# Kernel optimization log

Measured on AMD Instinct MI355X. Metric: run time of the kernel, lower is better.

## Reference

```python
import jax, jax.numpy as jnp
import numpy as np
import math

MAX_P = 150
D_MODEL = 128
N_HEADS = 4
D_HEAD = D_MODEL // N_HEADS
D_MLP = 512
D_MEM = 64
VOCAB = MAX_P + 2  # 152
EQ_TOKEN = MAX_P + 1  # 151
B = 65536


def setup_inputs() -> dict:
    key = jax.random.key(0)
    ks = jax.random.split(key, 20)
    s = 1.0 / math.sqrt(D_MODEL)
    inp = {
        "p_val": jax.random.randint(ks[0], (B,), 0, MAX_P),
        "a": jax.random.randint(ks[1], (B,), 0, MAX_P),
        "b": jax.random.randint(ks[2], (B,), 0, MAX_P),
        # embeddings
        "token_embed": jax.random.normal(ks[3], (VOCAB, D_MODEL), jnp.float32),
        "pos_embed": jax.random.normal(ks[4], (5, D_MODEL), jnp.float32),
        # TitansMemory
        "W_mem": jax.random.normal(ks[5], (D_MODEL, D_MEM), jnp.float32) * s,
        "b_mem": jnp.zeros((D_MEM,), jnp.float32),
        "W_sur": jax.random.normal(ks[6], (D_MEM, D_MODEL), jnp.float32) * (1.0 / math.sqrt(D_MEM)),
        "b_sur": jnp.zeros((D_MODEL,), jnp.float32),
        "W_m2r": jax.random.normal(ks[7], (D_MEM, D_MODEL), jnp.float32) * (1.0 / math.sqrt(D_MEM)),
        "b_m2r": jnp.zeros((D_MODEL,), jnp.float32),
        # attention
        "W_Q": jax.random.normal(ks[8], (N_HEADS, D_MODEL, D_HEAD), jnp.float32) * s,
        "W_K": jax.random.normal(ks[9], (N_HEADS, D_MODEL, D_HEAD), jnp.float32) * s,
        "W_V": jax.random.normal(ks[10], (N_HEADS, D_MODEL, D_HEAD), jnp.float32) * s,
        "W_O": jax.random.normal(ks[11], (N_HEADS, D_HEAD, D_MODEL), jnp.float32) * s,
        # MLP
        "W_mlp1": jax.random.normal(ks[12], (D_MODEL, D_MLP), jnp.float32) * s,
        "b_mlp1": jnp.zeros((D_MLP,), jnp.float32),
        "W_mlp2": jax.random.normal(ks[13], (D_MLP, D_MODEL), jnp.float32) * (1.0 / math.sqrt(D_MLP)),
        "b_mlp2": jnp.zeros((D_MODEL,), jnp.float32),
        # unembed
        "W_un": jax.random.normal(ks[14], (D_MODEL, MAX_P), jnp.float32) * s,
        "b_un": jnp.zeros((MAX_P,), jnp.float32),
    }
    return inp


def reference(p_val, a, b, token_embed, pos_embed, W_mem, b_mem, W_sur, b_sur,
              W_m2r, b_m2r, W_Q, W_K, W_V, W_O, W_mlp1, b_mlp1, W_mlp2, b_mlp2,
              W_un, b_un):
    eq = jnp.full_like(a, EQ_TOKEN)
    tokens = jnp.stack([p_val, a, b, eq], axis=1)            # [B, 4]
    x = token_embed[tokens] + pos_embed[:4][None, :, :]       # [B, 4, D]

    # Titans memory (test-time update) on the modulus token embedding
    x0 = x[:, 0, :]                                           # [B, D]
    z = jax.nn.silu(x0 @ W_mem + b_mem)                       # [B, d_mem]
    pred_x = z @ W_sur + b_sur                                # [B, D]
    update = jax.nn.silu((x0 - pred_x) @ W_mem)               # [B, d_mem]
    mem = (z + update) @ W_m2r + b_m2r                        # [B, D]
    x = x + mem[:, None, :]

    # attention
    q = jnp.einsum('bsd,hdk->bhsk', x, W_Q)
    k = jnp.einsum('bsd,hdk->bhsk', x, W_K)
    v = jnp.einsum('bsd,hdk->bhsk', x, W_V)
    scores = jnp.einsum('bhsk,bhtk->bhst', q, k) / math.sqrt(D_HEAD)
    pattern = jax.nn.softmax(scores, axis=-1)                 # [B, H, 4, 4]
    attn = jnp.einsum('bhst,bhtk->bhsk', pattern, v)
    attn = jnp.einsum('bhsk,hkm->bsm', attn, W_O)             # [B, 4, D]
    x = x + attn

    # MLP
    x = x + jax.nn.relu(x @ W_mlp1 + b_mlp1) @ W_mlp2 + b_mlp2

    # unembed the '=' position
    logits = x[:, 3, :] @ W_un + b_un                         # [B, max_p]
    return logits
```

## Files before the change

kernel.cpp:

```cpp
#include <hip/hip_runtime.h>

#define D      128
#define DM     64
#define DMLP   512
#define PMAX   150
#define VOC    152
#define EQT    151
#define NBATCH 65536

typedef __attribute__((ext_vector_type(8))) __bf16 bf16x8;
typedef __attribute__((ext_vector_type(4))) float  f32x4;

__device__ __forceinline__ float silu_f(float x){ return x / (1.0f + expf(-x)); }

#define OFF_MEMVEC 0
#define OFF_X3BASE 19200
#define OFF_KE     19328
#define OFF_KP     38784
#define OFF_SC     39296
#define OFF_O0     132896
#define OFF_O1     171296
#define OFF_O2     209696
#define OFF_O3     248096
#define OFF_M3B    248352
#define OFF_W1F    257952
#define OFF_W2F    290720
#define OFF_WUF    323488

__global__ void k_P1a(const float* __restrict__ tok, const float* __restrict__ pos,
                      const float* __restrict__ W_mem, const float* __restrict__ b_mem,
                      const float* __restrict__ W_sur, const float* __restrict__ b_sur,
                      const float* __restrict__ W_m2r, const float* __restrict__ b_m2r,
                      const float* __restrict__ W_K,
                      float* __restrict__ memvec, float* __restrict__ x3base,
                      float* __restrict__ KE, float* __restrict__ KP)
{
    int r = blockIdx.x, t = threadIdx.x;
    if (r < 150) {
        int p = r;
        __shared__ float sx0[D], sz[DM], sdiff[D], szu[DM];
        if (t < D) sx0[t] = tok[p*D + t] + pos[t];
        __syncthreads();
        if (t < DM) {
            float acc = b_mem[t];
            for (int d = 0; d < D; d++) acc += sx0[d] * W_mem[d*DM + t];
            sz[t] = silu_f(acc);
        }
        __syncthreads();
        if (t < D) {
            float acc = b_sur[t];
            for (int j = 0; j < DM; j++) acc += sz[j] * W_sur[j*D + t];
            sdiff[t] = sx0[t] - acc;
        }
        __syncthreads();
        if (t < DM) {
            float acc = 0.f;
            for (int d = 0; d < D; d++) acc += sdiff[d] * W_mem[d*DM + t];
            szu[t] = sz[t] + silu_f(acc);
        }
        __syncthreads();
        if (t < D) {
            float acc = b_m2r[t];
            for (int j = 0; j < DM; j++) acc += szu[j] * W_m2r[j*D + t];
            memvec[p*D + t] = acc;
        }
    } else if (r == 150) {
        if (t < D) x3base[t] = tok[EQT*D + t] + pos[3*D + t];
    } else {
        int idx = r - 151;
        const float* src = (idx < 152) ? (tok + idx*D) : (pos + (idx-152)*D);
        float*       dst = (idx < 152) ? (KE + idx*D)  : (KP + (idx-152)*D);
        __shared__ float s[D];
        if (t < D) s[t] = src[t];
        __syncthreads();
        if (t < D) {
            int h = t >> 5, k = t & 31;
            float acc = 0.f;
            for (int d = 0; d < D; d++) acc += s[d] * W_K[h*4096 + d*32 + k];
            dst[t] = acc;
        }
    }
}

__global__ void k_P2x(const float* __restrict__ memvec, const float* __restrict__ x3base,
                      const float* __restrict__ W_Q, const float* __restrict__ W_V,
                      const float* __restrict__ W_O,
                      const float* __restrict__ KE, const float* __restrict__ KP,
                      const float* __restrict__ tok, const float* __restrict__ pos,
                      const float* __restrict__ W1, const float* __restrict__ W2,
                      const float* __restrict__ WU,
                      float* __restrict__ SC, __bf16* __restrict__ M3B,
                      __bf16* __restrict__ O0, __bf16* __restrict__ O1,
                      __bf16* __restrict__ O2, __bf16* __restrict__ O3,
                      __bf16* __restrict__ W1f, __bf16* __restrict__ W2f, __bf16* __restrict__ WUf)
{
    int r = blockIdx.x, t = threadIdx.x;
    if (r < 300) {
        int p = r >> 1, half = r & 1;
        __shared__ float sMem[D], sIn[D], sQ3[D], sMV[D];
        if (t < D) { float m = memvec[p*D + t]; sMem[t] = m; sIn[t] = m + x3base[t]; }
        __syncthreads();
        if (t < D) {
            int h = t >> 5, k = t & 31;
            float acc = 0.f;
            for (int d = 0; d < D; d++) acc += sIn[d] * W_Q[h*4096 + d*32 + k];
            sQ3[t] = acc;
        } else {
            int c = t - D; int h = c >> 5, k = c & 31;
            float acc = 0.f;
            for (int d = 0; d < D; d++) acc += sMem[d] * W_V[h*4096 + d*32 + k];
            sMV[c] = acc;
        }
        __syncthreads();
        const float scale = 0.17677669529663687f;
        for (int ii = t; ii < 312; ii += 256) {
            int i = half*312 + ii;
            int v = i >> 2, h = i & 3;
            const float4* qh = (const float4*)(sQ3 + h*32);
            float4 s4 = {0.f, 0.f, 0.f, 0.f};
            if (v < 152) {
                const float4* ke = (const float4*)(KE + v*D + h*32);
                #pragma unroll
                for (int k = 0; k < 8; k++) {
                    float4 q = qh[k], e = ke[k];
                    s4.x += q.x*e.x; s4.y += q.y*e.y; s4.z += q.z*e.z; s4.w += q.w*e.w;
                }
            } else if (v == 152 || v == 153) {
                const float4* ke = (const float4*)(KE + ((v==152)? p : EQT)*D + h*32);
                const float4* kp = (const float4*)(KP + ((v==152)? 0 : 3)*D + h*32);
                #pragma unroll
                for (int k = 0; k < 8; k++) {
                    float4 q = qh[k], e = ke[k], pp = kp[k];
                    s4.x += q.x*(e.x+pp.x); s4.y += q.y*(e.y+pp.y);
                    s4.z += q.z*(e.z+pp.z); s4.w += q.w*(e.w+pp.w);
                }
            } else {
                const float4* kp = (const float4*)(KP + ((v==154)?1:2)*D + h*32);
                #pragma unroll
                for (int k = 0; k < 8; k++) {
                    float4 q = qh[k], pp = kp[k];
                    s4.x += q.x*pp.x; s4.y += q.y*pp.y; s4.z += q.z*pp.z; s4.w += q.w*pp.w;
                }
            }
            SC[p*624 + i] = (s4.x + s4.y + s4.z + s4.w) * scale;
        }
        if (half == 0 && t < D) {
            float acc = sIn[t];
            for (int c = 0; c < D; c++) acc += sMV[c] * W_O[c*D + t];
            M3B[p*D + t] = (__bf16)acc;
        }
        return;
    }
    int rr = r - 300;
    if (rr < 451) {
        int idx = rr;
        int tt, v; __bf16* outp;
        if (idx < 150)      { tt = 0; v = idx;       outp = O0 + v*512; }
        else if (idx < 300) { tt = 1; v = idx - 150; outp = O1 + (idx-150)*512; }
        else if (idx < 450) { tt = 2; v = idx - 300; outp = O2 + (idx-300)*512; }
        else                { tt = 3; v = EQT;       outp = O3; }
        __shared__ float sTP[D], sv[D];
        if (t < D) sTP[t] = tok[v*D + t] + pos[tt*D + t];
        __syncthreads();
        if (t < D) {
            int h = t >> 5, k = t & 31;
            float acc = 0.f;
            for (int d = 0; d < D; d++) acc += sTP[d] * W_V[h*4096 + d*32 + k];
            sv[t] = acc;
        }
        __syncthreads();
        #pragma unroll
        for (int i = 0; i < 2; i++) {
            int c = t + i*256;
            int h = c >> 7, m = c & 127;
            float acc = 0.f;
            for (int k = 0; k < 32; k++) acc += sv[h*32 + k] * W_O[h*4096 + k*128 + m];
            outp[c] = (__bf16)acc;
        }
    } else if (rr < 483) {
        int f = (rr-451)*256 + t;
        int l = f & 63, kb = (f>>6) & 3, nb = f >> 8;
        int k0 = kb*32 + (l>>4)*8, n = nb*16 + (l&15);
        #pragma unroll
        for (int j = 0; j < 8; j++) W1f[f*8 + j] = (__bf16)W1[(k0+j)*DMLP + n];
    } else if (rr < 515) {
        int f = (rr-483)*256 + t;
        int l = f & 63, g = f >> 6;
        int nb = g & 7, kb = g >> 3;
        int k0 = kb*32 + (l>>4)*8, n = nb*16 + (l&15);
        #pragma unroll
        for (int j = 0; j < 8; j++) W2f[f*8 + j] = (__bf16)W2[(k0+j)*D + n];
    } else {
        int f = (rr-515)*256 + t;
        int l = f & 63, kb = (f>>6) & 3, nb = f >> 8;
        int k0 = kb*32 + (l>>4)*8, n = nb*16 + (l&15);
        #pragma unroll
        for (int j = 0; j < 8; j++) WUf[f*8 + j] = (__bf16)((n < 150) ? WU[(k0+j)*150 + n] : 0.f);
    }
}

__global__ __launch_bounds__(256, 2) void k_fused(
    const int* __restrict__ p_val, const int* __restrict__ a_tok, const int* __restrict__ b_tok,
    const float* __restrict__ SC, const __bf16* __restrict__ O0, const __bf16* __restrict__ O1,
    const __bf16* __restrict__ O2, const __bf16* __restrict__ O3g, const __bf16* __restrict__ M3B,
    const __bf16* __restrict__ W1f, const __bf16* __restrict__ W2f, const __bf16* __restrict__ WUf,
    const float* __restrict__ b1, const float* __restrict__ b2, const float* __restrict__ bun,
    float* __restrict__ out)
{
    __shared__ __align__(16) char smem[54400];
    float* sB = (float*)(smem + 51200);
    char* sX3 = smem;

    int tid = threadIdx.x;
    int wv = tid >> 6, l = tid & 63, lr = l & 15, quad = l >> 4;
    int tbase = blockIdx.x * 128 + wv * 32;

    const char* gW1 = (const char*)W1f;
    const char* gW2 = (const char*)W2f;

    float4 v0, v1, v2, v3;
    {
        const float4* g1 = (const float4*)gW1;
        const float4* g2 = (const float4*)gW2;
        v0 = g1[tid]; v1 = g1[tid + 256]; v2 = g2[tid]; v3 = g2[tid + 256];
    }

    for (int i = tid; i < 512; i += 256) sB[i] = b1[i];
    if (tid < 128) sB[512 + tid] = b2[tid];
    if (tid < 160) sB[640 + tid] = bun[tid];

    #pragma unroll
    for (int ss = 0; ss < 2; ss++) {
        int s = (tid >> 2) + ss*64, h = tid & 3;
        int gs = blockIdx.x * 128 + s;
        int p = p_val[gs], ta = a_tok[gs], tb = b_tok[gs];

        float wloc[4];
        {
            const float* SCp = SC + p*624;
            float sc0 = SCp[608 + h];
            float sc3 = SCp[612 + h];
            float sc1 = SCp[ta*4 + h] + SCp[616 + h];
            float sc2 = SCp[tb*4 + h] + SCp[620 + h];
            float mx = fmaxf(fmaxf(sc0, sc1), fmaxf(sc2, sc3));
            float e0 = expf(sc0-mx), e1 = expf(sc1-mx), e2 = expf(sc2-mx), e3 = expf(sc3-mx);
            float inv = 1.f / (e0 + e1 + e2 + e3);
            wloc[0] = e0*inv; wloc[1] = e1*inv; wloc[2] = e2*inv; wloc[3] = e3*inv;
        }
        float w[16];
        #pragma unroll
        for (int j = 0; j < 4; j++) w[h*4 + j] = wloc[j];
        #pragma unroll
        for (int m = 1; m < 4; m++) {
            int oh = h ^ m;
            #pragma unroll
            for (int j = 0; j < 4; j++) w[oh*4 + j] = __shfl_xor(wloc[j], m);
        }

        const bf16x8* m3v = (const bf16x8*)(M3B + p*128);
        const bf16x8* t0  = (const bf16x8*)(O0 + p*512);
        const bf16x8* t1  = (const bf16x8*)(O1 + ta*512);
        const bf16x8* t2  = (const bf16x8*)(O2 + tb*512);
        const bf16x8* t3  = (const bf16x8*)O3g;
        #pragma unroll
        for (int jj = 0; jj < 4; jj++) {
            int c8 = h*4 + jj;
            bf16x8 mv = m3v[c8];
            float v[8];
            #pragma unroll
            for (int e = 0; e < 8; e++) v[e] = (float)mv[e];
            #pragma unroll
            for (int hh = 0; hh < 4; hh++) {
                int o8 = hh*16 + c8;
                bf16x8 e0 = t0[o8], e1 = t1[o8], e2 = t2[o8], e3 = t3[o8];
                float w0 = w[hh*4+0], w1 = w[hh*4+1], w2 = w[hh*4+2], w3 = w[hh*4+3];
                #pragma unroll
                for (int e = 0; e < 8; e++)
                    v[e] += w0*(float)e0[e] + w1*(float)e1[e] + w2*(float)e2[e] + w3*(float)e3[e];
            }
            bf16x8 st;
            #pragma unroll
            for (int e = 0; e < 8; e++) st[e] = (__bf16)v[e];
            *(bf16x8*)(sX3 + s*256 + ((c8*16) ^ ((s&7)<<4))) = st;
        }
    }
    __syncthreads();

    bf16x8 a[2][4];
    #pragma unroll
    for (int rg = 0; rg < 2; rg++) {
        int arow = wv*32 + rg*16 + lr;
        #pragma unroll
        for (int kb = 0; kb < 4; kb++)
            a[rg][kb] = *(const bf16x8*)(sX3 + arow*256 + ((kb*64 + quad*16) ^ ((lr&7)<<4)));
    }
    __syncthreads();

    char* sPanC = smem + 16384 + wv*2560;

    f32x4 acc2[2][8];
    #pragma unroll
    for (int rg = 0; rg < 2; rg++)
        #pragma unroll
        for (int i = 0; i < 8; i++) acc2[rg][i] = (f32x4){0.f, 0.f, 0.f, 0.f};

    for (int cc = 0; cc < 16; cc++) {
        {
            float4* d1 = (float4*)smem;
            float4* d2 = (float4*)(smem + 8192);
            d1[tid] = v0; d1[tid + 256] = v1; d2[tid] = v2; d2[tid + 256] = v3;
        }
        __syncthreads();
        if (cc < 15) {
            const float4* g1 = (const float4*)(gW1 + (cc+1)*8192);
            const float4* g2 = (const float4*)(gW2 + (cc+1)*8192);
            v0 = g1[tid]; v1 = g1[tid + 256]; v2 = g2[tid]; v3 = g2[tid + 256];
        }
        #pragma unroll
        for (int nbl = 0; nbl < 2; nbl++) {
            float bv = sB[cc*32 + nbl*16 + lr];
            f32x4 accA = (f32x4){bv, bv, bv, bv};
            f32x4 accB = (f32x4){bv, bv, bv, bv};
            #pragma unroll
            for (int kb = 0; kb < 4; kb++) {
                bf16x8 w1 = *(const bf16x8*)(smem + ((nbl*4 + kb)*64 + l)*16);
                accA = __builtin_amdgcn_mfma_f32_16x16x32_bf16(a[0][kb], w1, accA, 0, 0, 0);
                accB = __builtin_amdgcn_mfma_f32_16x16x32_bf16(a[1][kb], w1, accB, 0, 0, 0);
            }
            #pragma unroll
            for (int r = 0; r < 4; r++) {
                *(__bf16*)(sPanC + (((quad*4 + r)*40)      + nbl*16 + lr)*2) = (__bf16)fmaxf(accA[r], 0.f);
                *(__bf16*)(sPanC + (((16 + quad*4 + r)*40) + nbl*16 + lr)*2) = (__bf16)fmaxf(accB[r], 0.f);
            }
        }
        {
            bf16x8 h0 = *(const bf16x8*)(sPanC + ((lr)*40      + quad*8)*2);
            bf16x8 h1 = *(const bf16x8*)(sPanC + ((16 + lr)*40 + quad*8)*2);
            #pragma unroll
            for (int nb2 = 0; nb2 < 8; nb2++) {
                bf16x8 w2 = *(const bf16x8*)(smem + 8192 + (nb2*64 + l)*16);
                acc2[0][nb2] = __builtin_amdgcn_mfma_f32_16x16x32_bf16(h0, w2, acc2[0][nb2], 0, 0, 0);
                acc2[1][nb2] = __builtin_amdgcn_mfma_f32_16x16x32_bf16(h1, w2, acc2[1][nb2], 0, 0, 0);
            }
        }
        __syncthreads();
    }

    #pragma unroll
    for (int nb2 = 0; nb2 < 8; nb2++) {
        int kb = nb2 >> 1;
        bf16x8 bi;
        #pragma unroll
        for (int j = 0; j < 8; j++)
            bi[j] = (kb*32 + quad*8 + j == nb2*16 + lr) ? (__bf16)1.0f : (__bf16)0.0f;
        acc2[0][nb2] = __builtin_amdgcn_mfma_f32_16x16x32_bf16(a[0][kb], bi, acc2[0][nb2], 0, 0, 0);
        acc2[1][nb2] = __builtin_amdgcn_mfma_f32_16x16x32_bf16(a[1][kb], bi, acc2[1][nb2], 0, 0, 0);
    }

    char* sPanE = smem + 16384 + wv*8704;
    #pragma unroll
    for (int nb2 = 0; nb2 < 8; nb2++) {
        int n = nb2*16 + lr;
        float bv = sB[512 + n];
        #pragma unroll
        for (int rg = 0; rg < 2; rg++)
            #pragma unroll
            for (int r = 0; r < 4; r++) {
                float v = acc2[rg][nb2][r] + bv;
                *(__bf16*)(sPanE + (((rg*16 + quad*4 + r)*136) + n)*2) = (__bf16)v;
            }
    }
    bf16x8 au[2][4];
    #pragma unroll
    for (int rg = 0; rg < 2; rg++)
        #pragma unroll
        for (int kb = 0; kb < 4; kb++)
            au[rg][kb] = *(const bf16x8*)(sPanE + ((rg*16 + lr)*136 + kb*32 + quad*8)*2);

    const char* gWU = (const char*)WUf;
    #pragma unroll
    for (int q = 0; q < 3; q++) {
        if (q < 2) {
            const float4* g = (const float4*)(gWU + q*16384);
            float4 u0 = g[tid], u1 = g[tid+256], u2 = g[tid+512], u3 = g[tid+768];
            float4* dd = (float4*)smem;
            dd[tid] = u0; dd[tid+256] = u1; dd[tid+512] = u2; dd[tid+768] = u3;
        } else {
            const float4* g = (const float4*)(gWU + 32768);
            float4 u0 = g[tid], u1 = g[tid+256];
            float4* dd = (float4*)smem;
            dd[tid] = u0; dd[tid+256] = u1;
        }
        __syncthreads();
        int ntn = (q < 2) ? 4 : 2;
        for (int ntl = 0; ntl < ntn; ntl++) {
            int nt = q*4 + ntl;
            int n = nt*16 + lr;
            float bv = (n < 150) ? sB[640 + n] : 0.f;
            f32x4 accU0 = (f32x4){bv, bv, bv, bv};
            f32x4 accU1 = (f32x4){bv, bv, bv, bv};
            #pragma unroll
            for (int kb = 0; kb < 4; kb++) {
                bf16x8 wu = *(const bf16x8*)(smem + ((ntl*4 + kb)*64 + l)*16);
                accU0 = __builtin_amdgcn_mfma_f32_16x16x32_bf16(au[0][kb], wu, accU0, 0, 0, 0);
                accU1 = __builtin_amdgcn_mfma_f32_16x16x32_bf16(au[1][kb], wu, accU1, 0, 0, 0);
            }
            if (n < 150) {
                #pragma unroll
                for (int r = 0; r < 4; r++) {
                    out[(tbase +      quad*4 + r)*150 + n] = accU0[r];
                    out[(tbase + 16 + quad*4 + r)*150 + n] = accU1[r];
                }
            }
        }
        if (q < 2) __syncthreads();
    }
}

extern "C" void kernel_launch(void* const* d_in, const int* in_sizes, int n_in,
                              void* d_out, int out_size, void* d_ws, size_t ws_size,
                              hipStream_t stream) {
    const int*   p_val = (const int*)d_in[0];
    const int*   a_tok = (const int*)d_in[1];
    const int*   b_tok = (const int*)d_in[2];
    const float* tok   = (const float*)d_in[3];
    const float* pos   = (const float*)d_in[4];
    const float* W_mem = (const float*)d_in[5];
    const float* b_mem = (const float*)d_in[6];
    const float* W_sur = (const float*)d_in[7];
    const float* b_sur = (const float*)d_in[8];
    const float* W_m2r = (const float*)d_in[9];
    const float* b_m2r = (const float*)d_in[10];
    const float* W_Q   = (const float*)d_in[11];
    const float* W_K   = (const float*)d_in[12];
    const float* W_V   = (const float*)d_in[13];
    const float* W_O   = (const float*)d_in[14];
    const float* W1    = (const float*)d_in[15];
    const float* b1    = (const float*)d_in[16];
    const float* W2    = (const float*)d_in[17];
    const float* b2    = (const float*)d_in[18];
    const float* WU    = (const float*)d_in[19];
    const float* bun   = (const float*)d_in[20];
    float* out = (float*)d_out;

    float* ws = (float*)d_ws;
    float* memvec = ws + OFF_MEMVEC;
    float* x3base = ws + OFF_X3BASE;
    float* KE     = ws + OFF_KE;
    float* KP     = ws + OFF_KP;
    float* SC     = ws + OFF_SC;
    __bf16* O0    = (__bf16*)(ws + OFF_O0);
    __bf16* O1    = (__bf16*)(ws + OFF_O1);
    __bf16* O2    = (__bf16*)(ws + OFF_O2);
    __bf16* O3    = (__bf16*)(ws + OFF_O3);
    __bf16* M3B   = (__bf16*)(ws + OFF_M3B);
    __bf16* W1f   = (__bf16*)(ws + OFF_W1F);
    __bf16* W2f   = (__bf16*)(ws + OFF_W2F);
    __bf16* WUf   = (__bf16*)(ws + OFF_WUF);

    k_P1a<<<307, 256, 0, stream>>>(tok, pos, W_mem, b_mem, W_sur, b_sur, W_m2r, b_m2r,
                                   W_K, memvec, x3base, KE, KP);
    k_P2x<<<825, 256, 0, stream>>>(memvec, x3base, W_Q, W_V, W_O, KE, KP,
                                   tok, pos, W1, W2, WU,
                                   SC, M3B, O0, O1, O2, O3, W1f, W2f, WUf);
    k_fused<<<NBATCH/128, 256, 0, stream>>>(p_val, a_tok, b_tok, SC, O0, O1, O2, O3, M3B,
                                            W1f, W2f, WUf, b1, b2, bun, out);
}
```

Before: 179.3 us.

## Double-buffer MLP weight chunks in LDS and drop shared bias staging

Splits the W1/W2 chunk staging into two LDS buffers, so the next chunk is written after the current chunk's MFMAs and each loop iteration needs one barrier instead of two. X3 rows are now assigned per wave, so each wave reads back only its own rows and the barrier before the A-fragment load goes away. Biases are read directly from global memory rather than staged in LDS, and the LDS footprint shrinks to 48KB. The cost is extra global bias loads inside the loop and reliance on explicit waitcnt and sched barriers for correctness.

```diff
diff --git a/kernel.cpp b/kernel.cpp
--- a/kernel.cpp
+++ b/kernel.cpp
@@ -207,9 +207,8 @@
     const float* __restrict__ b1, const float* __restrict__ b2, const float* __restrict__ bun,
     float* __restrict__ out)
 {
-    __shared__ __align__(16) char smem[54400];
-    float* sB = (float*)(smem + 51200);
-    char* sX3 = smem;
+    __shared__ __align__(16) char smem[49152];
+    char* sX3 = smem + 8192;
 
     int tid = threadIdx.x;
     int wv = tid >> 6, l = tid & 63, lr = l & 15, quad = l >> 4;
@@ -225,14 +224,11 @@
         v0 = g1[tid]; v1 = g1[tid + 256]; v2 = g2[tid]; v3 = g2[tid + 256];
     }
 
-    for (int i = tid; i < 512; i += 256) sB[i] = b1[i];
-    if (tid < 128) sB[512 + tid] = b2[tid];
-    if (tid < 160) sB[640 + tid] = bun[tid];
-
     #pragma unroll
     for (int ss = 0; ss < 2; ss++) {
-        int s = (tid >> 2) + ss*64, h = tid & 3;
-        int gs = blockIdx.x * 128 + s;
+        int sl = l >> 2, h = l & 3;
+        int row = wv*32 + ss*16 + sl;
+        int gs = blockIdx.x * 128 + row;
         int p = p_val[gs], ta = a_tok[gs], tb = b_tok[gs];
 
         float wloc[4];
@@ -281,10 +277,9 @@
             bf16x8 st;
             #pragma unroll
             for (int e = 0; e < 8; e++) st[e] = (__bf16)v[e];
-            *(bf16x8*)(sX3 + s*256 + ((c8*16) ^ ((s&7)<<4))) = st;
-        }
-    }
-    __syncthreads();
+            *(bf16x8*)(sX3 + row*256 + ((c8*16) ^ ((row&7)<<4))) = st;
+        }
+    }
 
     bf16x8 a[2][4];
     #pragma unroll
@@ -292,11 +287,23 @@
         int arow = wv*32 + rg*16 + lr;
         #pragma unroll
         for (int kb = 0; kb < 4; kb++)
-            a[rg][kb] = *(const bf16x8*)(sX3 + arow*256 + ((kb*64 + quad*16) ^ ((lr&7)<<4)));
+            a[rg][kb] = *(const bf16x8*)(sX3 + arow*256 + ((kb*64 + quad*16) ^ ((arow&7)<<4)));
+    }
+    asm volatile("s_waitcnt lgkmcnt(0)" ::: "memory");
+    __builtin_amdgcn_sched_barrier(0);
+
+    {
+        float4* d1 = (float4*)smem;
+        d1[tid] = v0; d1[tid + 256] = v1;
     }
     __syncthreads();
-
-    char* sPanC = smem + 16384 + wv*2560;
+    {
+        float4* d2 = (float4*)(smem + 16384);
+        d2[tid] = v2; d2[tid + 256] = v3;
+    }
+    __syncthreads();
+
+    char* sPanH = smem + 32768 + wv*2560;
 
     f32x4 acc2[2][8];
     #pragma unroll
@@ -305,12 +312,9 @@
         for (int i = 0; i < 8; i++) acc2[rg][i] = (f32x4){0.f, 0.f, 0.f, 0.f};
 
     for (int cc = 0; cc < 16; cc++) {
-        {
-            float4* d1 = (float4*)smem;
-            float4* d2 = (float4*)(smem + 8192);
-            d1[tid] = v0; d1[tid + 256] = v1; d2[tid] = v2; d2[tid + 256] = v3;
-        }
-        __syncthreads();
+        int p = cc & 1;
+        char* w1b = smem + p*8192;
+        char* w2b = smem + 16384 + p*8192;
         if (cc < 15) {
             const float4* g1 = (const float4*)(gW1 + (cc+1)*8192);
             const float4* g2 = (const float4*)(gW2 + (cc+1)*8192);
@@ -318,30 +322,35 @@
         }
         #pragma unroll
         for (int nbl = 0; nbl < 2; nbl++) {
-            float bv = sB[cc*32 + nbl*16 + lr];
+            float bv = b1[cc*32 + nbl*16 + lr];
             f32x4 accA = (f32x4){bv, bv, bv, bv};
             f32x4 accB = (f32x4){bv, bv, bv, bv};
             #pragma unroll
             for (int kb = 0; kb < 4; kb++) {
-                bf16x8 w1 = *(const bf16x8*)(smem + ((nbl*4 + kb)*64 + l)*16);
+                bf16x8 w1 = *(const bf16x8*)(w1b + ((nbl*4 + kb)*64 + l)*16);
                 accA = __builtin_amdgcn_mfma_f32_16x16x32_bf16(a[0][kb], w1, accA, 0, 0, 0);
                 accB = __builtin_amdgcn_mfma_f32_16x16x32_bf16(a[1][kb], w1, accB, 0, 0, 0);
             }
             #pragma unroll
             for (int r = 0; r < 4; r++) {
-                *(__bf16*)(sPanC + (((quad*4 + r)*40)      + nbl*16 + lr)*2) = (__bf16)fmaxf(accA[r], 0.f);
-                *(__bf16*)(sPanC + (((16 + quad*4 + r)*40) + nbl*16 + lr)*2) = (__bf16)fmaxf(accB[r], 0.f);
+                *(__bf16*)(sPanH + (((quad*4 + r)*40)      + nbl*16 + lr)*2) = (__bf16)fmaxf(accA[r], 0.f);
+                *(__bf16*)(sPanH + (((16 + quad*4 + r)*40) + nbl*16 + lr)*2) = (__bf16)fmaxf(accB[r], 0.f);
             }
         }
         {
-            bf16x8 h0 = *(const bf16x8*)(sPanC + ((lr)*40      + quad*8)*2);
-            bf16x8 h1 = *(const bf16x8*)(sPanC + ((16 + lr)*40 + quad*8)*2);
+            bf16x8 h0 = *(const bf16x8*)(sPanH + ((lr)*40      + quad*8)*2);
+            bf16x8 h1 = *(const bf16x8*)(sPanH + ((16 + lr)*40 + quad*8)*2);
             #pragma unroll
             for (int nb2 = 0; nb2 < 8; nb2++) {
-                bf16x8 w2 = *(const bf16x8*)(smem + 8192 + (nb2*64 + l)*16);
+                bf16x8 w2 = *(const bf16x8*)(w2b + (nb2*64 + l)*16);
                 acc2[0][nb2] = __builtin_amdgcn_mfma_f32_16x16x32_bf16(h0, w2, acc2[0][nb2], 0, 0, 0);
                 acc2[1][nb2] = __builtin_amdgcn_mfma_f32_16x16x32_bf16(h1, w2, acc2[1][nb2], 0, 0, 0);
             }
+        }
+        if (cc < 15) {
+            float4* d1 = (float4*)(smem + (p^1)*8192);
+            float4* d2 = (float4*)(smem + 16384 + (p^1)*8192);
+            d1[tid] = v0; d1[tid + 256] = v1; d2[tid] = v2; d2[tid + 256] = v3;
         }
         __syncthreads();
     }
@@ -357,38 +366,44 @@
         acc2[1][nb2] = __builtin_amdgcn_mfma_f32_16x16x32_bf16(a[1][kb], bi, acc2[1][nb2], 0, 0, 0);
     }
 
-    char* sPanE = smem + 16384 + wv*8704;
     #pragma unroll
     for (int nb2 = 0; nb2 < 8; nb2++) {
         int n = nb2*16 + lr;
-        float bv = sB[512 + n];
+        float bv = b2[n];
         #pragma unroll
         for (int rg = 0; rg < 2; rg++)
             #pragma unroll
             for (int r = 0; r < 4; r++) {
                 float v = acc2[rg][nb2][r] + bv;
-                *(__bf16*)(sPanE + (((rg*16 + quad*4 + r)*136) + n)*2) = (__bf16)v;
-            }
-    }
+                int row = wv*32 + rg*16 + quad*4 + r;
+                *(__bf16*)(smem + row*256 + ((n*2) ^ ((row&7)<<4))) = (__bf16)v;
+            }
+    }
+    asm volatile("s_waitcnt lgkmcnt(0)" ::: "memory");
+    __builtin_amdgcn_sched_barrier(0);
     bf16x8 au[2][4];
     #pragma unroll
-    for (int rg = 0; rg < 2; rg++)
+    for (int rg = 0; rg < 2; rg++) {
+        int arow = wv*32 + rg*16 + lr;
         #pragma unroll
         for (int kb = 0; kb < 4; kb++)
-            au[rg][kb] = *(const bf16x8*)(sPanE + ((rg*16 + lr)*136 + kb*32 + quad*8)*2);
+            au[rg][kb] = *(const bf16x8*)(smem + arow*256 + ((kb*64 + quad*16) ^ ((arow&7)<<4)));
+    }
 
     const char* gWU = (const char*)WUf;
+    char* sWU = smem + 32768;
     #pragma unroll
     for (int q = 0; q < 3; q++) {
+        __syncthreads();
         if (q < 2) {
             const float4* g = (const float4*)(gWU + q*16384);
             float4 u0 = g[tid], u1 = g[tid+256], u2 = g[tid+512], u3 = g[tid+768];
-            float4* dd = (float4*)smem;
+            float4* dd = (float4*)sWU;
             dd[tid] = u0; dd[tid+256] = u1; dd[tid+512] = u2; dd[tid+768] = u3;
         } else {
             const float4* g = (const float4*)(gWU + 32768);
             float4 u0 = g[tid], u1 = g[tid+256];
-            float4* dd = (float4*)smem;
+            float4* dd = (float4*)sWU;
             dd[tid] = u0; dd[tid+256] = u1;
         }
         __syncthreads();
@@ -396,12 +411,12 @@
         for (int ntl = 0; ntl < ntn; ntl++) {
             int nt = q*4 + ntl;
             int n = nt*16 + lr;
-            float bv = (n < 150) ? sB[640 + n] : 0.f;
+            float bv = (n < 150) ? bun[n] : 0.f;
             f32x4 accU0 = (f32x4){bv, bv, bv, bv};
             f32x4 accU1 = (f32x4){bv, bv, bv, bv};
             #pragma unroll
             for (int kb = 0; kb < 4; kb++) {
-                bf16x8 wu = *(const bf16x8*)(smem + ((ntl*4 + kb)*64 + l)*16);
+                bf16x8 wu = *(const bf16x8*)(sWU + ((ntl*4 + kb)*64 + l)*16);
                 accU0 = __builtin_amdgcn_mfma_f32_16x16x32_bf16(au[0][kb], wu, accU0, 0, 0, 0);
                 accU1 = __builtin_amdgcn_mfma_f32_16x16x32_bf16(au[1][kb], wu, accU1, 0, 0, 0);
             }
@@ -413,7 +428,6 @@
                 }
             }
         }
-        if (q < 2) __syncthreads();
     }
 }
 
```

New measurement: 180.4 us. Within noise of the previous version (+0.6%).
